# Kernel tuning notes

Measured on AMD Instinct MI355X. Metric: run time of the kernel, lower is better.

The kernel has to match this reference:

```python
import jax, jax.numpy as jnp
import numpy as np
import math

D_MODEL = 2048
Q_HEAD = 32
KV_HEAD = 8
HEAD_DIM = D_MODEL // Q_HEAD  # 64
GROUP = Q_HEAD // KV_HEAD     # 4
B, T = 2, 2048


def setup_inputs() -> dict:
    key = jax.random.key(0)
    ks = jax.random.split(key, 9)
    s = 0.02
    return {
        "x": jax.random.normal(ks[0], (B, T, D_MODEL), dtype=jnp.float32),
        "Wq": jax.random.normal(ks[1], (D_MODEL, Q_HEAD * HEAD_DIM), dtype=jnp.float32) * s,
        "bq": jnp.zeros((Q_HEAD * HEAD_DIM,), dtype=jnp.float32),
        "Wk": jax.random.normal(ks[2], (D_MODEL, KV_HEAD * HEAD_DIM), dtype=jnp.float32) * s,
        "bk": jnp.zeros((KV_HEAD * HEAD_DIM,), dtype=jnp.float32),
        "Wv": jax.random.normal(ks[3], (D_MODEL, KV_HEAD * HEAD_DIM), dtype=jnp.float32) * s,
        "bv": jnp.zeros((KV_HEAD * HEAD_DIM,), dtype=jnp.float32),
        "Wo": jax.random.normal(ks[4], (D_MODEL, D_MODEL), dtype=jnp.float32) * s,
        "bo": jnp.zeros((D_MODEL,), dtype=jnp.float32),
    }


def reference(x, Wq, bq, Wk, bk, Wv, bv, Wo, bo):
    Bx, Tx, C = x.shape
    # projections -> [B, H, T, Dh]
    q = (x @ Wq + bq).reshape(Bx, Tx, Q_HEAD, HEAD_DIM).transpose(0, 2, 1, 3)
    k = (x @ Wk + bk).reshape(Bx, Tx, KV_HEAD, HEAD_DIM).transpose(0, 2, 1, 3)
    v = (x @ Wv + bv).reshape(Bx, Tx, KV_HEAD, HEAD_DIM).transpose(0, 2, 1, 3)
    # GQA: repeat each KV head `GROUP` times (repeat_interleave semantics)
    k = jnp.repeat(k, GROUP, axis=1)
    v = jnp.repeat(v, GROUP, axis=1)
    score = jnp.einsum("bhqd,bhkd->bhqk", q, k) / math.sqrt(HEAD_DIM)
    causal = jnp.tril(jnp.ones((Tx, Tx), dtype=bool))
    score = jnp.where(causal, score, -jnp.inf)
    attn = jax.nn.softmax(score, axis=-1)
    out = jnp.einsum("bhqk,bhkd->bhqd", attn, v)
    out = out.transpose(0, 2, 1, 3).reshape(Bx, Tx, C)
    return out @ Wo + bo
```

## Files before the change

kernel.cpp:

```cpp
#include <hip/hip_runtime.h>
#include <hip/hip_bf16.h>

typedef unsigned short u16;
typedef __attribute__((ext_vector_type(8)))  __bf16 bf16x8;
typedef __attribute__((ext_vector_type(8)))  unsigned short u16x8;
typedef __attribute__((ext_vector_type(4)))  unsigned short u16x4;
typedef __attribute__((ext_vector_type(4)))  float f32x4;
typedef __attribute__((ext_vector_type(16))) float f32x16;
typedef __attribute__((ext_vector_type(4)))  unsigned u32x4;

#define MFMA(a, b, c)   __builtin_amdgcn_mfma_f32_16x16x32_bf16((a), (b), (c), 0, 0, 0)
#define MFMA32(a, b, c) __builtin_amdgcn_mfma_f32_32x32x16_bf16((a), (b), (c), 0, 0, 0)

__device__ __forceinline__ u16 f2b(float f) {
  union { float f; unsigned u; } x; x.f = f;
  unsigned r = x.u + 0x7fffu + ((x.u >> 16) & 1u);
  return (u16)(r >> 16);
}

__device__ __forceinline__ unsigned pack2(float lo, float hi) {
  const __bf16 a = (__bf16)lo, b = (__bf16)hi;
  return (unsigned)__builtin_bit_cast(u16, a) | ((unsigned)__builtin_bit_cast(u16, b) << 16);
}

__device__ __forceinline__ bf16x8 ld2x64(const u16* p) {
  union { u16x4 h[2]; bf16x8 v; } u;
  u.h[0] = *(const u16x4*)p;
  u.h[1] = *(const u16x4*)(p + 4);
  return u.v;
}

__device__ __forceinline__ void gl_lds16(void* lds, const void* g) {
  __builtin_amdgcn_global_load_lds(
      (const __attribute__((address_space(1))) void*)g,
      (__attribute__((address_space(3))) void*)lds, 16, 0, 0);
}

__global__ __launch_bounds__(256) void cvt_kernel(const float* __restrict__ in,
                                                  u16* __restrict__ out, int n) {
  int i = (blockIdx.x * 256 + threadIdx.x) * 4;
  if (i >= n) return;
  f32x4 v = *(const f32x4*)(in + i);
  u16x4 o;
  o[0] = f2b(v[0]); o[1] = f2b(v[1]); o[2] = f2b(v[2]); o[3] = f2b(v[3]);
  *(u16x4*)(out + i) = o;
}

__global__ __launch_bounds__(256) void cvt_t_kernel(const float* __restrict__ W,
                                                    u16* __restrict__ Wt, int K, int N) {
  __shared__ u16 t[32][36];
  const int n0 = blockIdx.x * 32, k0 = blockIdx.y * 32;
  const int r = threadIdx.x >> 3, c4 = (threadIdx.x & 7) * 4;
  f32x4 v = *(const f32x4*)&W[(size_t)(k0 + r) * N + n0 + c4];
  t[c4 + 0][r] = f2b(v[0]);
  t[c4 + 1][r] = f2b(v[1]);
  t[c4 + 2][r] = f2b(v[2]);
  t[c4 + 3][r] = f2b(v[3]);
  __syncthreads();
  u16x4 o;
  o[0] = t[r][c4]; o[1] = t[r][c4 + 1]; o[2] = t[r][c4 + 2]; o[3] = t[r][c4 + 3];
  *(u16x4*)&Wt[(size_t)(n0 + r) * K + k0 + c4] = o;
}

template <bool OUT_BF16>
__device__ __forceinline__ void gemm_body(const u16* __restrict__ A, const u16* __restrict__ Bt,
                                          const float* __restrict__ bias, void* __restrict__ C,
                                          const int N, const int n0, const int m0, const float scale) {
  __shared__ __align__(16) u16 As[128 * 32];
  __shared__ __align__(16) u16 Bs[128 * 32];
  const int tid = threadIdx.x;
  const int lane = tid & 63, wv = tid >> 6;
  const int l15 = lane & 15, lg = lane >> 4;
  const int wm = wv >> 2, wn = wv & 3;
  const int srow = tid >> 2;
  const int g = tid & 3;
  const int gs = g ^ ((srow >> 1) & 3);

  f32x4 acc[4][2] = {};

  for (int k0 = 0; k0 < 2048; k0 += 32) {
    gl_lds16(&As[wv << 9], A  + (((size_t)(m0 + srow)) << 11) + k0 + gs * 8);
    gl_lds16(&Bs[wv << 9], Bt + (((size_t)(n0 + srow)) << 11) + k0 + gs * 8);
    __syncthreads();
    bf16x8 af[4], bfr[2];
#pragma unroll
    for (int t = 0; t < 4; t++) {
      const int ra = wm * 64 + t * 16 + l15;
      af[t] = *(const bf16x8*)&As[ra * 32 + ((lg ^ ((ra >> 1) & 3)) << 3)];
    }
#pragma unroll
    for (int u = 0; u < 2; u++) {
      const int rb = wn * 32 + u * 16 + l15;
      bfr[u] = *(const bf16x8*)&Bs[rb * 32 + ((lg ^ ((rb >> 1) & 3)) << 3)];
    }
#pragma unroll
    for (int mt = 0; mt < 4; mt++)
#pragma unroll
      for (int nt = 0; nt < 2; nt++)
        acc[mt][nt] = MFMA(af[mt], bfr[nt], acc[mt][nt]);
    __syncthreads();
  }

#pragma unroll
  for (int nt = 0; nt < 2; nt++) {
    const int col = n0 + wn * 32 + nt * 16 + l15;
    const float bc = bias[col];
#pragma unroll
    for (int mt = 0; mt < 4; mt++) {
#pragma unroll
      for (int r = 0; r < 4; r++) {
        const int row = m0 + wm * 64 + mt * 16 + lg * 4 + r;
        const float v = (acc[mt][nt][r] + bc) * scale;
        if (OUT_BF16) ((u16*)C)[(size_t)row * N + col] = f2b(v);
        else          ((float*)C)[(size_t)row * N + col] = v;
      }
    }
  }
}

__global__ __launch_bounds__(512, 6) void qkv_gemm_kernel(
    const u16* __restrict__ xb,
    const u16* __restrict__ Wqt, const u16* __restrict__ Wkt, const u16* __restrict__ Wvt,
    const float* __restrict__ bq, const float* __restrict__ bk, const float* __restrict__ bv,
    u16* __restrict__ Qb, u16* __restrict__ Kb, u16* __restrict__ Vb) {
  const int nb = blockIdx.x;
  const u16* Bt; const float* bias; u16* out; int N, n0; float scale;
  if (nb < 16)      { Bt = Wqt; bias = bq; out = Qb; N = 2048; n0 = nb * 128;        scale = 0.125f * 1.44269504f; }
  else if (nb < 20) { Bt = Wkt; bias = bk; out = Kb; N = 512;  n0 = (nb - 16) * 128; scale = 1.0f; }
  else              { Bt = Wvt; bias = bv; out = Vb; N = 512;  n0 = (nb - 20) * 128; scale = 1.0f; }
  gemm_body<true>(xb, Bt, bias, out, N, n0, blockIdx.y * 128, scale);
}

__global__ __launch_bounds__(512, 6) void oproj_kernel(const u16* __restrict__ Ab,
                                                       const u16* __restrict__ Wot,
                                                       const float* __restrict__ bo,
                                                       float* __restrict__ out) {
  gemm_body<false>(Ab, Wot, bo, out, 2048, blockIdx.x * 128, blockIdx.y * 128, 1.0f);
}

__global__ __launch_bounds__(512, 4) void attn_kernel(const u16* __restrict__ Qb,
                                                      const u16* __restrict__ Kb,
                                                      const u16* __restrict__ Vb,
                                                      u16* __restrict__ Ab) {
  const int i = blockIdx.x;
  const int j = i & 255;
  const int kh = j & 7, b = (j >> 3) & 1;
  const int p16 = j >> 4;
  const int qt = (i < 256) ? (31 - p16) : p16;

  const int tid = threadIdx.x;
  const int lane = tid & 63, wv = tid >> 6;
  const int hh = wv & 3, qh = wv >> 2;
  const int h = kh * 4 + hh;
  const int l31 = lane & 31, hi = lane >> 5;
  const int swz = (l31 & 7) << 3;

  __shared__ __align__(16) u16 Ks[2][64 * 64];
  __shared__ __align__(16) u16 Vt[2][64 * 68];

  const int skv = tid >> 3;
  const int sc8 = tid & 7;
  const int sd0 = sc8 * 8;

  const u16* Kbase = Kb + (size_t)(b * 2048) * 512 + kh * 64;
  const u16* Vbase = Vb + (size_t)(b * 2048) * 512 + kh * 64;

  const int q0 = qt * 64;

  bf16x8 qf[4];
  {
    const u16* qp = Qb + (size_t)(b * 2048 + q0 + qh * 32 + l31) * 2048 + h * 64 + hi * 8;
#pragma unroll
    for (int c = 0; c < 4; c++) qf[c] = *(const bf16x8*)(qp + c * 16);
  }
  f32x16 ot[2] = {};
  float mrow = -30000.0f, srow = 0.f;

  int cur = 0;
  {
    gl_lds16(&Ks[0][wv << 9], Kbase + ((size_t)skv << 9) + ((sc8 ^ (skv & 7)) << 3));
    u16x8 vr = *(const u16x8*)(Vbase + ((size_t)skv << 9) + sd0);
#pragma unroll
    for (int j8 = 0; j8 < 8; j8++) {
      const int jj = (j8 + sc8) & 7;
      const int d = sd0 + jj;
      Vt[0][d * 68 + skv] = vr[jj];
    }
  }
  for (int it = 0; it <= qt; ++it) {
    __syncthreads();
    const bool pre = (it < qt);
    u16x8 vnx;
    if (pre) {
      const size_t roff = (size_t)((it + 1) * 64 + skv) << 9;
      gl_lds16(&Ks[cur ^ 1][wv << 9], Kbase + roff + ((sc8 ^ (skv & 7)) << 3));
      vnx = *(const u16x8*)(Vbase + roff + sd0);
    }
    const u16* Kc = Ks[cur];
    const u16* Vc = Vt[cur];

    f32x16 sc2[2] = {};
#pragma unroll
    for (int c = 0; c < 4; c++) {
      const int dblk = (c * 16 + hi * 8) ^ swz;
#pragma unroll
      for (int kvh = 0; kvh < 2; kvh++) {
        bf16x8 kf = *(const bf16x8*)&Kc[(kvh * 32 + l31) * 64 + dblk];
        sc2[kvh] = MFMA32(kf, qf[c], sc2[kvh]);
      }
    }
    if (it == qt) {
      const int q = qh * 32 + l31;
#pragma unroll
      for (int kvh = 0; kvh < 2; kvh++)
#pragma unroll
        for (int r = 0; r < 16; r++) {
          const int kv = kvh * 32 + (r & 3) + 8 * (r >> 2) + 4 * hi;
          if (kv > q) sc2[kvh][r] = -30000.0f;
        }
    }
    float tm = fmaxf(sc2[0][0], sc2[0][1]);
#pragma unroll
    for (int kvh = 0; kvh < 2; kvh++)
#pragma unroll
      for (int r = (kvh ? 0 : 2); r < 16; r++) tm = fmaxf(tm, sc2[kvh][r]);
    tm = fmaxf(tm, __shfl_xor(tm, 32));
    if (__any(tm > mrow + 8.0f)) {
      const float mnew = fmaxf(mrow, tm);
      const float scl = __builtin_amdgcn_exp2f(mrow - mnew);
      mrow = mnew;
      srow *= scl;
#pragma unroll
      for (int dh = 0; dh < 2; dh++)
#pragma unroll
        for (int r = 0; r < 16; r++) ot[dh][r] *= scl;
    }
    float ps = 0.f;
#pragma unroll
    for (int kvh = 0; kvh < 2; kvh++) {
      unsigned pk[8];
#pragma unroll
      for (int j8 = 0; j8 < 8; j8++) {
        const float p0 = __builtin_amdgcn_exp2f(sc2[kvh][2 * j8] - mrow);
        const float p1 = __builtin_amdgcn_exp2f(sc2[kvh][2 * j8 + 1] - mrow);
        ps += p0 + p1;
        pk[j8] = pack2(p0, p1);
      }
#pragma unroll
      for (int tt = 0; tt < 2; tt++) {
        const int t = kvh * 2 + tt;
        const unsigned a0 = pk[4 * tt + 0], a1 = pk[4 * tt + 1];
        const unsigned b0 = pk[4 * tt + 2], b1 = pk[4 * tt + 3];
        const unsigned s0 = hi ? a0 : b0, s1 = hi ? a1 : b1;
        const unsigned r0 = (unsigned)__shfl_xor((int)s0, 32);
        const unsigned r1 = (unsigned)__shfl_xor((int)s1, 32);
        u32x4 pw;
        pw[0] = hi ? r0 : a0;
        pw[1] = hi ? r1 : a1;
        pw[2] = hi ? b0 : r0;
        pw[3] = hi ? b1 : r1;
        const bf16x8 pf = __builtin_bit_cast(bf16x8, pw);
#pragma unroll
        for (int dh = 0; dh < 2; dh++) {
          bf16x8 vf = ld2x64(&Vc[(dh * 32 + l31) * 68 + t * 16 + hi * 8]);
          ot[dh] = MFMA32(vf, pf, ot[dh]);
        }
      }
    }
    ps += __shfl_xor(ps, 32);
    srow += ps;
    if (pre) {
#pragma unroll
      for (int j8 = 0; j8 < 8; j8++) {
        const int jj = (j8 + sc8) & 7;
        const int d = sd0 + jj;
        Vt[cur ^ 1][d * 68 + skv] = vnx[jj];
      }
    }
    cur ^= 1;
  }
  __syncthreads();
  u16* Sx = (wv < 4) ? &Ks[0][0] + wv * 2048 : &Vt[0][0] + (wv - 4) * 2048;
  const float inv = 1.0f / srow;
#pragma unroll
  for (int dh = 0; dh < 2; dh++)
#pragma unroll
    for (int jr = 0; jr < 8; jr++) {
      const unsigned w = pack2(ot[dh][2 * jr] * inv, ot[dh][2 * jr + 1] * inv);
      const int d = dh * 32 + 8 * (jr >> 1) + (jr & 1) * 2 + 4 * hi;
      *(unsigned*)&Sx[l31 * 64 + (d ^ swz)] = w;
    }
  __syncthreads();
#pragma unroll
  for (int rep = 0; rep < 4; rep++) {
    const int chunk = rep * 64 + lane;
    const int qr = chunk >> 3, cc = chunk & 7;
    u16x8 val = *(const u16x8*)&Sx[qr * 64 + ((cc * 8) ^ ((qr & 7) << 3))];
    *(u16x8*)&Ab[(size_t)(b * 2048 + q0 + qh * 32 + qr) * 2048 + h * 64 + cc * 8] = val;
  }
}

extern "C" void kernel_launch(void* const* d_in, const int* in_sizes, int n_in,
                              void* d_out, int out_size, void* d_ws, size_t ws_size,
                              hipStream_t stream) {
  const float* x  = (const float*)d_in[0];
  const float* Wq = (const float*)d_in[1];
  const float* bq = (const float*)d_in[2];
  const float* Wk = (const float*)d_in[3];
  const float* bk = (const float*)d_in[4];
  const float* Wv = (const float*)d_in[5];
  const float* bv = (const float*)d_in[6];
  const float* Wo = (const float*)d_in[7];
  const float* bo = (const float*)d_in[8];

  char* ws = (char*)d_ws;
  u16* xb  = (u16*)(ws + 0);
  u16* Ab  = (u16*)(ws + 0);
  u16* Qb  = (u16*)(ws + 16777216);
  u16* Kb  = (u16*)(ws + 33554432);
  u16* Vb  = (u16*)(ws + 37748736);
  u16* Wqt = (u16*)(ws + 41943040);
  u16* Wkt = (u16*)(ws + 50331648);
  u16* Wvt = (u16*)(ws + 52428800);
  u16* Wot = (u16*)(ws + 54525952);

  cvt_kernel<<<8192, 256, 0, stream>>>(x, xb, 2 * 2048 * 2048);
  cvt_t_kernel<<<dim3(64, 64), 256, 0, stream>>>(Wq, Wqt, 2048, 2048);
  cvt_t_kernel<<<dim3(16, 64), 256, 0, stream>>>(Wk, Wkt, 2048, 512);
  cvt_t_kernel<<<dim3(16, 64), 256, 0, stream>>>(Wv, Wvt, 2048, 512);
  cvt_t_kernel<<<dim3(64, 64), 256, 0, stream>>>(Wo, Wot, 2048, 2048);

  qkv_gemm_kernel<<<dim3(24, 32), 512, 0, stream>>>(xb, Wqt, Wkt, Wvt, bq, bk, bv, Qb, Kb, Vb);
  attn_kernel<<<dim3(512), 512, 0, stream>>>(Qb, Kb, Vb, Ab);
  oproj_kernel<<<dim3(16, 32), 512, 0, stream>>>(Ab, Wot, bo, (float*)d_out);
}
```

Baseline: 214.2 us.

## Split attention blocks to two heads per block and merge weight conversion launches

The attention kernel now uses 256-thread blocks that each cover two of the four query heads in a KV group, doubling the grid to 1024 blocks. Each thread loads two K/V chunks per tile to fill the shared tiles. The intent is finer-grained scheduling of causal work and more resident blocks per CU, at the cost of each K/V tile being loaded twice (once per head pair). The four weight transpose-convert launches are also merged into one launch to cut launch overhead.

```diff
diff --git a/kernel.cpp b/kernel.cpp
--- a/kernel.cpp
+++ b/kernel.cpp
@@ -46,10 +46,19 @@
   *(u16x4*)(out + i) = o;
 }
 
-__global__ __launch_bounds__(256) void cvt_t_kernel(const float* __restrict__ W,
-                                                    u16* __restrict__ Wt, int K, int N) {
+__global__ __launch_bounds__(256) void cvt_t_all_kernel(
+    const float* __restrict__ Wq, const float* __restrict__ Wk,
+    const float* __restrict__ Wv, const float* __restrict__ Wo,
+    u16* __restrict__ Wqt, u16* __restrict__ Wkt,
+    u16* __restrict__ Wvt, u16* __restrict__ Wot) {
   __shared__ u16 t[32][36];
-  const int n0 = blockIdx.x * 32, k0 = blockIdx.y * 32;
+  const int x = blockIdx.x;
+  const float* W; u16* Wt; int N, n0;
+  if (x < 64)      { W = Wq; Wt = Wqt; N = 2048; n0 = x * 32; }
+  else if (x < 80) { W = Wk; Wt = Wkt; N = 512;  n0 = (x - 64) * 32; }
+  else if (x < 96) { W = Wv; Wt = Wvt; N = 512;  n0 = (x - 80) * 32; }
+  else             { W = Wo; Wt = Wot; N = 2048; n0 = (x - 96) * 32; }
+  const int k0 = blockIdx.y * 32;
   const int r = threadIdx.x >> 3, c4 = (threadIdx.x & 7) * 4;
   f32x4 v = *(const f32x4*)&W[(size_t)(k0 + r) * N + n0 + c4];
   t[c4 + 0][r] = f2b(v[0]);
@@ -59,7 +68,7 @@
   __syncthreads();
   u16x4 o;
   o[0] = t[r][c4]; o[1] = t[r][c4 + 1]; o[2] = t[r][c4 + 2]; o[3] = t[r][c4 + 3];
-  *(u16x4*)&Wt[(size_t)(n0 + r) * K + k0 + c4] = o;
+  *(u16x4*)&Wt[(size_t)(n0 + r) * 2048 + k0 + c4] = o;
 }
 
 template <bool OUT_BF16>
@@ -138,29 +147,25 @@
   gemm_body<false>(Ab, Wot, bo, out, 2048, blockIdx.x * 128, blockIdx.y * 128, 1.0f);
 }
 
-__global__ __launch_bounds__(512, 4) void attn_kernel(const u16* __restrict__ Qb,
+__global__ __launch_bounds__(256, 4) void attn_kernel(const u16* __restrict__ Qb,
                                                       const u16* __restrict__ Kb,
                                                       const u16* __restrict__ Vb,
                                                       u16* __restrict__ Ab) {
   const int i = blockIdx.x;
-  const int j = i & 255;
-  const int kh = j & 7, b = (j >> 3) & 1;
-  const int p16 = j >> 4;
-  const int qt = (i < 256) ? (31 - p16) : p16;
+  const int j = i & 511;
+  const int hp = j & 1, kh = (j >> 1) & 7, b = (j >> 4) & 1;
+  const int p16 = j >> 5;
+  const int qt = (i < 512) ? (31 - p16) : p16;
 
   const int tid = threadIdx.x;
   const int lane = tid & 63, wv = tid >> 6;
-  const int hh = wv & 3, qh = wv >> 2;
-  const int h = kh * 4 + hh;
+  const int hh = wv & 1, qh = wv >> 1;
+  const int h = kh * 4 + hp * 2 + hh;
   const int l31 = lane & 31, hi = lane >> 5;
   const int swz = (l31 & 7) << 3;
 
   __shared__ __align__(16) u16 Ks[2][64 * 64];
   __shared__ __align__(16) u16 Vt[2][64 * 68];
-
-  const int skv = tid >> 3;
-  const int sc8 = tid & 7;
-  const int sd0 = sc8 * 8;
 
   const u16* Kbase = Kb + (size_t)(b * 2048) * 512 + kh * 64;
   const u16* Vbase = Vb + (size_t)(b * 2048) * 512 + kh * 64;
@@ -178,23 +183,35 @@
 
   int cur = 0;
   {
-    gl_lds16(&Ks[0][wv << 9], Kbase + ((size_t)skv << 9) + ((sc8 ^ (skv & 7)) << 3));
-    u16x8 vr = *(const u16x8*)(Vbase + ((size_t)skv << 9) + sd0);
-#pragma unroll
-    for (int j8 = 0; j8 < 8; j8++) {
-      const int jj = (j8 + sc8) & 7;
-      const int d = sd0 + jj;
-      Vt[0][d * 68 + skv] = vr[jj];
+#pragma unroll
+    for (int s = 0; s < 2; s++) {
+      const int cid = s * 256 + tid;
+      const int row = cid >> 3, c8 = cid & 7;
+      gl_lds16(&Ks[0][s * 2048 + (wv << 9)],
+               Kbase + ((size_t)row << 9) + ((c8 ^ (row & 7)) << 3));
+      u16x8 vr = *(const u16x8*)(Vbase + ((size_t)row << 9) + c8 * 8);
+#pragma unroll
+      for (int j8 = 0; j8 < 8; j8++) {
+        const int jj = (j8 + c8) & 7;
+        const int d = c8 * 8 + jj;
+        Vt[0][d * 68 + row] = vr[jj];
+      }
     }
   }
   for (int it = 0; it <= qt; ++it) {
     __syncthreads();
     const bool pre = (it < qt);
-    u16x8 vnx;
+    u16x8 vnx[2];
     if (pre) {
-      const size_t roff = (size_t)((it + 1) * 64 + skv) << 9;
-      gl_lds16(&Ks[cur ^ 1][wv << 9], Kbase + roff + ((sc8 ^ (skv & 7)) << 3));
-      vnx = *(const u16x8*)(Vbase + roff + sd0);
+#pragma unroll
+      for (int s = 0; s < 2; s++) {
+        const int cid = s * 256 + tid;
+        const int row = cid >> 3, c8 = cid & 7;
+        const size_t roff = (size_t)((it + 1) * 64 + row) << 9;
+        gl_lds16(&Ks[cur ^ 1][s * 2048 + (wv << 9)],
+                 Kbase + roff + ((c8 ^ (row & 7)) << 3));
+        vnx[s] = *(const u16x8*)(Vbase + roff + c8 * 8);
+      }
     }
     const u16* Kc = Ks[cur];
     const u16* Vc = Vt[cur];
@@ -271,16 +288,21 @@
     srow += ps;
     if (pre) {
 #pragma unroll
-      for (int j8 = 0; j8 < 8; j8++) {
-        const int jj = (j8 + sc8) & 7;
-        const int d = sd0 + jj;
-        Vt[cur ^ 1][d * 68 + skv] = vnx[jj];
+      for (int s = 0; s < 2; s++) {
+        const int cid = s * 256 + tid;
+        const int row = cid >> 3, c8 = cid & 7;
+#pragma unroll
+        for (int j8 = 0; j8 < 8; j8++) {
+          const int jj = (j8 + c8) & 7;
+          const int d = c8 * 8 + jj;
+          Vt[cur ^ 1][d * 68 + row] = vnx[s][jj];
+        }
       }
     }
     cur ^= 1;
   }
   __syncthreads();
-  u16* Sx = (wv < 4) ? &Ks[0][0] + wv * 2048 : &Vt[0][0] + (wv - 4) * 2048;
+  u16* Sx = &Ks[0][0] + wv * 2048;
   const float inv = 1.0f / srow;
 #pragma unroll
   for (int dh = 0; dh < 2; dh++)
@@ -325,12 +347,9 @@
   u16* Wot = (u16*)(ws + 54525952);
 
   cvt_kernel<<<8192, 256, 0, stream>>>(x, xb, 2 * 2048 * 2048);
-  cvt_t_kernel<<<dim3(64, 64), 256, 0, stream>>>(Wq, Wqt, 2048, 2048);
-  cvt_t_kernel<<<dim3(16, 64), 256, 0, stream>>>(Wk, Wkt, 2048, 512);
-  cvt_t_kernel<<<dim3(16, 64), 256, 0, stream>>>(Wv, Wvt, 2048, 512);
-  cvt_t_kernel<<<dim3(64, 64), 256, 0, stream>>>(Wo, Wot, 2048, 2048);
+  cvt_t_all_kernel<<<dim3(160, 64), 256, 0, stream>>>(Wq, Wk, Wv, Wo, Wqt, Wkt, Wvt, Wot);
 
   qkv_gemm_kernel<<<dim3(24, 32), 512, 0, stream>>>(xb, Wqt, Wkt, Wvt, bq, bk, bv, Qb, Kb, Vb);
-  attn_kernel<<<dim3(512), 512, 0, stream>>>(Qb, Kb, Vb, Ab);
+  attn_kernel<<<dim3(1024), 256, 0, stream>>>(Qb, Kb, Vb, Ab);
   oproj_kernel<<<dim3(16, 32), 512, 0, stream>>>(Ab, Wot, bo, (float*)d_out);
 }
```

Result: slower. 219.9 us (+2.7%).
